# Kernel tuning notes

Measured on AMD Instinct MI355X. Metric: run time of the kernel, lower is better.

Reference implementation:

```python
import jax, jax.numpy as jnp
import numpy as np

DIM = 1024
HEADS = 16
DIM_HEAD = DIM // HEADS  # 64


def setup_inputs() -> dict:
    key = jax.random.key(0)
    k1, k2, k3 = jax.random.split(key, 3)
    x = jax.random.normal(k1, (4, 2048, DIM), dtype=jnp.float32)
    # Linear weights stored as [in, out] so y = x @ W (torch Linear uses x @ W.T; init is random either way)
    w_qkv = jax.random.normal(k2, (DIM, 3 * DIM), dtype=jnp.float32) * (DIM ** -0.5)
    w_out = jax.random.normal(k3, (DIM, DIM), dtype=jnp.float32) * (DIM ** -0.5)
    return {"x": x, "w_qkv": w_qkv, "w_out": w_out}


def reference(x, w_qkv, w_out):
    b, t, d = x.shape
    h, dh = HEADS, DIM_HEAD
    qkv = x @ w_qkv  # [b, t, 3*h*dh]
    q, k, v = jnp.split(qkv, 3, axis=-1)
    split_heads = lambda a: a.reshape(b, t, h, dh).transpose(0, 2, 1, 3)  # [b,h,t,dh]
    q, k, v = map(split_heads, (q, k, v))
    # NOTE: original scales by full model dim d, not per-head dim
    scale = d ** (-0.5)
    dots = jnp.einsum('bhie,bhje->bhij', q, k) * scale  # [b,h,t,t]
    attn = jax.nn.softmax(dots, axis=-1)
    out = jnp.einsum('bhij,bhje->bhie', attn, v)  # [b,h,t,dh]
    out = out.transpose(0, 2, 1, 3).reshape(b, t, h * dh)
    return out @ w_out
```

## Files before the change

kernel.cpp:

```cpp
#include <hip/hip_runtime.h>


typedef __bf16 bf16x8 __attribute__((ext_vector_type(8)));
typedef __bf16 bf16x4 __attribute__((ext_vector_type(4)));
typedef float f32x4 __attribute__((ext_vector_type(4)));
typedef unsigned short ushort8 __attribute__((ext_vector_type(8)));

#define MFMA16(a, b, c) __builtin_amdgcn_mfma_f32_16x16x32_bf16((a), (b), (c), 0, 0, 0)

__device__ __forceinline__ unsigned short f2bf(float f) {
  unsigned int u = __float_as_uint(f);
  u = (u + 0x7FFFu + ((u >> 16) & 1u)) >> 16;
  return (unsigned short)u;
}

__device__ __forceinline__ float fast_exp2(float x) {
#if __has_builtin(__builtin_amdgcn_exp2f)
  return __builtin_amdgcn_exp2f(x);
#else
  float r;
  asm("v_exp_f32 %0, %1" : "=v"(r) : "v"(x));
  return r;
#endif
}

__device__ __forceinline__ void gload_lds16(const unsigned short* g, unsigned short* l) {
  __builtin_amdgcn_global_load_lds(
      (const __attribute__((address_space(1))) unsigned int*)g,
      (__attribute__((address_space(3))) unsigned int*)l, 16, 0, 0);
}

__global__ __launch_bounds__(256) void cvt_f32_bf16(
    const float* __restrict__ in, unsigned short* __restrict__ out, int n) {
  int i = (blockIdx.x * 256 + threadIdx.x) * 8;
  if (i < n) {
    float4 a = *(const float4*)&in[i];
    float4 b = *(const float4*)&in[i + 4];
    ushort8 o = {f2bf(a.x), f2bf(a.y), f2bf(a.z), f2bf(a.w),
                 f2bf(b.x), f2bf(b.y), f2bf(b.z), f2bf(b.w)};
    *(ushort8*)&out[i] = o;
  }
}

__global__ __launch_bounds__(256) void transpose_f32_bf16(
    const float* __restrict__ in, unsigned short* __restrict__ out,
    int R, int C, int scale_limit, float scale) {
  __shared__ float t[32][33];
  const int c0 = blockIdx.x * 32, r0 = blockIdx.y * 32;
  const int tid = threadIdx.x;
#pragma unroll
  for (int i = 0; i < 4; ++i) {
    int e = tid + i * 256;
    int r = e >> 5, c = e & 31;
    t[r][c] = in[(size_t)(r0 + r) * C + c0 + c];
  }
  __syncthreads();
#pragma unroll
  for (int i = 0; i < 4; ++i) {
    int e = tid + i * 256;
    int r = e >> 5, c = e & 31;
    float v = t[c][r];
    if (c0 + r < scale_limit) v *= scale;
    out[(size_t)(c0 + r) * R + r0 + c] = f2bf(v);
  }
}

__global__ __launch_bounds__(256) void extract_vt(
    const unsigned short* __restrict__ qkv, unsigned short* __restrict__ VT) {
  const int bh = blockIdx.y, b = bh >> 4, h = bh & 15;
  const int t0 = blockIdx.x * 32;
  __shared__ unsigned short tile[32][65];
  const int tid = threadIdx.x;
#pragma unroll
  for (int i = 0; i < 8; ++i) {
    int e = tid + i * 256;
    int r = e >> 6, c = e & 63;
    tile[r][c] = qkv[(size_t)(b * 2048 + t0 + r) * 3072 + 2048 + h * 64 + c];
  }
  __syncthreads();
#pragma unroll
  for (int i = 0; i < 8; ++i) {
    int e = tid + i * 256;
    int r = e >> 5, c = e & 31;
    VT[(size_t)bh * 131072 + (size_t)r * 2048 + t0 + c] = tile[c][r];
  }
}

template <bool OUT_F32>
__global__ __launch_bounds__(256) void gemm_bt(
    const unsigned short* __restrict__ A, const unsigned short* __restrict__ Bt,
    void* __restrict__ Cv, int M, int N, int K) {
  __shared__ unsigned short As[128 * 32];
  __shared__ unsigned short Bs[128 * 32];
  const int tid = threadIdx.x;
  const int wave = tid >> 6, lane = tid & 63;
  const int g = lane >> 4, ln = lane & 15;
  const int wm = wave >> 1, wn = wave & 1;
  const long bm = (long)blockIdx.y * 128;
  const long bn = (long)blockIdx.x * 128;

  f32x4 acc[4][4];
#pragma unroll
  for (int i = 0; i < 4; ++i)
#pragma unroll
    for (int j = 0; j < 4; ++j) acc[i][j] = (f32x4){0.f, 0.f, 0.f, 0.f};

  const int srow = wave * 32 + (lane >> 2);
  const int scol = (lane & 3) * 8;
  const unsigned short* gA0 = A + (bm + srow) * (long)K + scol;
  const unsigned short* gA1 = gA0 + 16 * (long)K;
  const unsigned short* gB0 = Bt + (bn + srow) * (long)K + scol;
  const unsigned short* gB1 = gB0 + 16 * (long)K;
  unsigned short* lA0 = &As[wave * 1024];
  unsigned short* lA1 = &As[wave * 1024 + 512];
  unsigned short* lB0 = &Bs[wave * 1024];
  unsigned short* lB1 = &Bs[wave * 1024 + 512];

  for (int k0 = 0; k0 < K; k0 += 32) {
    __syncthreads();
    gload_lds16(gA0 + k0, lA0);
    gload_lds16(gA1 + k0, lA1);
    gload_lds16(gB0 + k0, lB0);
    gload_lds16(gB1 + k0, lB1);
    __syncthreads();

    bf16x8 af[4], bfr[4];
#pragma unroll
    for (int i = 0; i < 4; ++i) {
      af[i]  = *(const bf16x8*)&As[(wm * 64 + i * 16 + ln) * 32 + g * 8];
      bfr[i] = *(const bf16x8*)&Bs[(wn * 64 + i * 16 + ln) * 32 + g * 8];
    }
    __builtin_amdgcn_s_setprio(1);
#pragma unroll
    for (int i = 0; i < 4; ++i)
#pragma unroll
      for (int j = 0; j < 4; ++j)
        acc[i][j] = MFMA16(af[i], bfr[j], acc[i][j]);
    __builtin_amdgcn_s_setprio(0);
  }

  const long crow = bm + wm * 64, ccol = bn + wn * 64;
#pragma unroll
  for (int i = 0; i < 4; ++i)
#pragma unroll
    for (int j = 0; j < 4; ++j)
#pragma unroll
      for (int r = 0; r < 4; ++r) {
        long idx = (crow + i * 16 + g * 4 + r) * (long)N + ccol + j * 16 + ln;
        if (OUT_F32)
          ((float*)Cv)[idx] = acc[i][j][r];
        else
          ((unsigned short*)Cv)[idx] = f2bf(acc[i][j][r]);
      }
}

__global__ __launch_bounds__(256, 4) void attn_kernel(
    const unsigned short* __restrict__ qkv, const unsigned short* __restrict__ VT,
    unsigned short* __restrict__ attn_out) {
  __shared__ unsigned short Ks[64][72];
  __shared__ unsigned short Vs[64][72];
  __shared__ unsigned short Ps[4][2][16][72];

  const int tid = threadIdx.x;
  const int wave = tid >> 6, lane = tid & 63;
  const int g = lane >> 4, ln = lane & 15;

  const int wg = (blockIdx.x & 7) * 128 + (blockIdx.x >> 3);
  const int bh = wg >> 4, qc = wg & 15;
  const int b = bh >> 4, h = bh & 15;
  const int q0 = qc * 128;

  bf16x8 qf[2][2];
#pragma unroll
  for (int qb = 0; qb < 2; ++qb) {
    size_t base =
        (size_t)(b * 2048 + q0 + wave * 32 + qb * 16 + ln) * 3072 + h * 64 + g * 8;
    qf[qb][0] = *(const bf16x8*)&qkv[base];
    qf[qb][1] = *(const bf16x8*)&qkv[base + 32];
  }

  f32x4 oacc[2][4];
#pragma unroll
  for (int qb = 0; qb < 2; ++qb)
#pragma unroll
    for (int m = 0; m < 4; ++m) oacc[qb][m] = (f32x4){0.f, 0.f, 0.f, 0.f};
  float lsum[2] = {0.f, 0.f};

  const int srow = tid >> 3;
  const int sch = (tid & 7) * 8;
  const unsigned short* gK =
      qkv + (size_t)b * 2048 * 3072 + 1024 + h * 64 + (size_t)srow * 3072 + sch;
  const unsigned short* gV = VT + (size_t)bh * 131072 + (size_t)srow * 2048 + sch;

  for (int j0 = 0; j0 < 2048; j0 += 64) {
    __syncthreads();
    *(ushort8*)&Ks[srow][sch]      = *(const ushort8*)(gK + (size_t)j0 * 3072);
    *(ushort8*)&Ks[srow + 32][sch] = *(const ushort8*)(gK + (size_t)(j0 + 32) * 3072);
    *(ushort8*)&Vs[srow][sch]      = *(const ushort8*)(gV + j0);
    *(ushort8*)&Vs[srow + 32][sch] = *(const ushort8*)(gV + 32 * 2048 + j0);
    __syncthreads();

    f32x4 sacc[2][4];
#pragma unroll
    for (int qb = 0; qb < 2; ++qb)
#pragma unroll
      for (int mb = 0; mb < 4; ++mb) sacc[qb][mb] = (f32x4){0.f, 0.f, 0.f, 0.f};
    __builtin_amdgcn_s_setprio(1);
#pragma unroll
    for (int mb = 0; mb < 4; ++mb) {
      bf16x8 kf0 = *(const bf16x8*)&Ks[mb * 16 + ln][g * 8];
      bf16x8 kf1 = *(const bf16x8*)&Ks[mb * 16 + ln][32 + g * 8];
#pragma unroll
      for (int qb = 0; qb < 2; ++qb) {
        sacc[qb][mb] = MFMA16(kf0, qf[qb][0], sacc[qb][mb]);
        sacc[qb][mb] = MFMA16(kf1, qf[qb][1], sacc[qb][mb]);
      }
    }
    __builtin_amdgcn_s_setprio(0);

#pragma unroll
    for (int qb = 0; qb < 2; ++qb) {
#pragma unroll
      for (int mb = 0; mb < 4; ++mb) {
        float p0 = fast_exp2(sacc[qb][mb][0]);
        float p1 = fast_exp2(sacc[qb][mb][1]);
        float p2 = fast_exp2(sacc[qb][mb][2]);
        float p3 = fast_exp2(sacc[qb][mb][3]);
        lsum[qb] += (p0 + p1) + (p2 + p3);
        bf16x4 pk = {(__bf16)p0, (__bf16)p1, (__bf16)p2, (__bf16)p3};
        *(bf16x4*)&Ps[wave][qb][ln][mb * 16 + g * 4] = pk;
      }
    }

    asm volatile("s_waitcnt lgkmcnt(0)" ::: "memory");

    bf16x8 pf[2][2];
#pragma unroll
    for (int qb = 0; qb < 2; ++qb) {
      pf[qb][0] = *(const bf16x8*)&Ps[wave][qb][ln][g * 8];
      pf[qb][1] = *(const bf16x8*)&Ps[wave][qb][ln][32 + g * 8];
    }
    __builtin_amdgcn_s_setprio(1);
#pragma unroll
    for (int mb = 0; mb < 4; ++mb) {
      bf16x8 vf0 = *(const bf16x8*)&Vs[mb * 16 + ln][g * 8];
      bf16x8 vf1 = *(const bf16x8*)&Vs[mb * 16 + ln][32 + g * 8];
#pragma unroll
      for (int qb = 0; qb < 2; ++qb) {
        oacc[qb][mb] = MFMA16(vf0, pf[qb][0], oacc[qb][mb]);
        oacc[qb][mb] = MFMA16(vf1, pf[qb][1], oacc[qb][mb]);
      }
    }
    __builtin_amdgcn_s_setprio(0);
  }

#pragma unroll
  for (int qb = 0; qb < 2; ++qb) {
    float l = lsum[qb];
    l += __shfl_xor(l, 16);
    l += __shfl_xor(l, 32);
    float inv = 1.0f / l;
    size_t row = (size_t)(b * 2048 + q0 + wave * 32 + qb * 16 + ln) * 1024 + h * 64;
#pragma unroll
    for (int mb = 0; mb < 4; ++mb) {
      bf16x4 o = {(__bf16)(oacc[qb][mb][0] * inv), (__bf16)(oacc[qb][mb][1] * inv),
                  (__bf16)(oacc[qb][mb][2] * inv), (__bf16)(oacc[qb][mb][3] * inv)};
      *(bf16x4*)&attn_out[row + mb * 16 + g * 4] = o;
    }
  }
}

extern "C" void kernel_launch(void* const* d_in, const int* in_sizes, int n_in,
                              void* d_out, int out_size, void* d_ws, size_t ws_size,
                              hipStream_t stream) {
  (void)in_sizes; (void)n_in; (void)out_size; (void)ws_size;
  const float* x_f     = (const float*)d_in[0];
  const float* w_qkv_f = (const float*)d_in[1];
  const float* w_out_f = (const float*)d_in[2];
  float* out = (float*)d_out;

  char* ws = (char*)d_ws;
  unsigned short* qkv   = (unsigned short*)(ws);
  unsigned short* attn  = (unsigned short*)(ws + 50331648);
  unsigned short* VT    = (unsigned short*)(ws + 67108864);
  unsigned short* WqkvT = (unsigned short*)(ws + 83886080);
  unsigned short* WoutT = (unsigned short*)(ws + 90177536);
  unsigned short* xb    = (unsigned short*)(ws + 92274688);

  const float kQScale = 0.045084220027780106f;

  cvt_f32_bf16<<<4096, 256, 0, stream>>>(x_f, xb, 8192 * 1024);
  transpose_f32_bf16<<<dim3(3072 / 32, 1024 / 32), 256, 0, stream>>>(
      w_qkv_f, WqkvT, 1024, 3072, 1024, kQScale);
  transpose_f32_bf16<<<dim3(1024 / 32, 1024 / 32), 256, 0, stream>>>(
      w_out_f, WoutT, 1024, 1024, 0, 1.0f);
  gemm_bt<false><<<dim3(3072 / 128, 8192 / 128), 256, 0, stream>>>(xb, WqkvT, qkv, 8192, 3072, 1024);
  extract_vt<<<dim3(64, 64), 256, 0, stream>>>(qkv, VT);
  attn_kernel<<<1024, 256, 0, stream>>>(qkv, VT, attn);
  gemm_bt<true><<<dim3(1024 / 128, 8192 / 128), 256, 0, stream>>>(attn, WoutT, out, 8192, 1024, 1024);
}
```

Baseline: 201.0 us.

## Fuse prep kernels and write V transposed directly from QKV GEMM epilogue

Merges the x conversion and both weight transposes into a single prep kernel, and removes the separate extract_vt pass by having the QKV GEMM epilogue write the V columns straight into the transposed VT layout. This removes three kernel launches and one full read/write pass over V. The attention row-sum accumulation is also changed to packed two-wide float adds. The VT epilogue stores are 8-byte strided writes, which may be less coalesced than the original row-major stores.

```diff
diff --git a/kernel.cpp b/kernel.cpp
--- a/kernel.cpp
+++ b/kernel.cpp
@@ -4,6 +4,7 @@
 typedef __bf16 bf16x8 __attribute__((ext_vector_type(8)));
 typedef __bf16 bf16x4 __attribute__((ext_vector_type(4)));
 typedef float f32x4 __attribute__((ext_vector_type(4)));
+typedef float f32x2 __attribute__((ext_vector_type(2)));
 typedef unsigned short ushort8 __attribute__((ext_vector_type(8)));
 
 #define MFMA16(a, b, c) __builtin_amdgcn_mfma_f32_16x16x32_bf16((a), (b), (c), 0, 0, 0)
@@ -30,24 +31,35 @@
       (__attribute__((address_space(3))) unsigned int*)l, 16, 0, 0);
 }
 
-__global__ __launch_bounds__(256) void cvt_f32_bf16(
-    const float* __restrict__ in, unsigned short* __restrict__ out, int n) {
-  int i = (blockIdx.x * 256 + threadIdx.x) * 8;
-  if (i < n) {
-    float4 a = *(const float4*)&in[i];
-    float4 b = *(const float4*)&in[i + 4];
+__global__ __launch_bounds__(256) void prep_kernel(
+    const float* __restrict__ x, unsigned short* __restrict__ xb,
+    const float* __restrict__ wqkv, unsigned short* __restrict__ WqkvT,
+    const float* __restrict__ wout, unsigned short* __restrict__ WoutT) {
+  const int bid = blockIdx.x;
+  const int tid = threadIdx.x;
+  if (bid < 4096) {
+    int i = (bid * 256 + tid) * 8;
+    float4 a = *(const float4*)&x[i];
+    float4 b = *(const float4*)&x[i + 4];
     ushort8 o = {f2bf(a.x), f2bf(a.y), f2bf(a.z), f2bf(a.w),
                  f2bf(b.x), f2bf(b.y), f2bf(b.z), f2bf(b.w)};
-    *(ushort8*)&out[i] = o;
-  }
-}
-
-__global__ __launch_bounds__(256) void transpose_f32_bf16(
-    const float* __restrict__ in, unsigned short* __restrict__ out,
-    int R, int C, int scale_limit, float scale) {
+    *(ushort8*)&xb[i] = o;
+    return;
+  }
   __shared__ float t[32][33];
-  const int c0 = blockIdx.x * 32, r0 = blockIdx.y * 32;
-  const int tid = threadIdx.x;
+  const float* in;
+  unsigned short* out;
+  int C, scale_limit, c0, r0;
+  if (bid < 4096 + 3072) {
+    int tj = bid - 4096;
+    in = wqkv; out = WqkvT; C = 3072; scale_limit = 1024;
+    c0 = (tj % 96) * 32; r0 = (tj / 96) * 32;
+  } else {
+    int tj = bid - 7168;
+    in = wout; out = WoutT; C = 1024; scale_limit = 0;
+    c0 = (tj & 31) * 32; r0 = (tj >> 5) * 32;
+  }
+  const float kQScale = 0.045084220027780106f;
 #pragma unroll
   for (int i = 0; i < 4; ++i) {
     int e = tid + i * 256;
@@ -60,36 +72,16 @@
     int e = tid + i * 256;
     int r = e >> 5, c = e & 31;
     float v = t[c][r];
-    if (c0 + r < scale_limit) v *= scale;
-    out[(size_t)(c0 + r) * R + r0 + c] = f2bf(v);
-  }
-}
-
-__global__ __launch_bounds__(256) void extract_vt(
-    const unsigned short* __restrict__ qkv, unsigned short* __restrict__ VT) {
-  const int bh = blockIdx.y, b = bh >> 4, h = bh & 15;
-  const int t0 = blockIdx.x * 32;
-  __shared__ unsigned short tile[32][65];
-  const int tid = threadIdx.x;
-#pragma unroll
-  for (int i = 0; i < 8; ++i) {
-    int e = tid + i * 256;
-    int r = e >> 6, c = e & 63;
-    tile[r][c] = qkv[(size_t)(b * 2048 + t0 + r) * 3072 + 2048 + h * 64 + c];
-  }
-  __syncthreads();
-#pragma unroll
-  for (int i = 0; i < 8; ++i) {
-    int e = tid + i * 256;
-    int r = e >> 5, c = e & 31;
-    VT[(size_t)bh * 131072 + (size_t)r * 2048 + t0 + c] = tile[c][r];
-  }
-}
-
-template <bool OUT_F32>
+    if (c0 + r < scale_limit) v *= kQScale;
+    out[(size_t)(c0 + r) * 1024 + r0 + c] = f2bf(v);
+  }
+}
+
+template <int MODE>
 __global__ __launch_bounds__(256) void gemm_bt(
     const unsigned short* __restrict__ A, const unsigned short* __restrict__ Bt,
-    void* __restrict__ Cv, int M, int N, int K) {
+    void* __restrict__ Cv, unsigned short* __restrict__ VT,
+    int M, int N, int K) {
   __shared__ unsigned short As[128 * 32];
   __shared__ unsigned short Bs[128 * 32];
   const int tid = threadIdx.x;
@@ -140,18 +132,34 @@
   }
 
   const long crow = bm + wm * 64, ccol = bn + wn * 64;
-#pragma unroll
-  for (int i = 0; i < 4; ++i)
-#pragma unroll
-    for (int j = 0; j < 4; ++j)
-#pragma unroll
-      for (int r = 0; r < 4; ++r) {
-        long idx = (crow + i * 16 + g * 4 + r) * (long)N + ccol + j * 16 + ln;
-        if (OUT_F32)
-          ((float*)Cv)[idx] = acc[i][j][r];
-        else
-          ((unsigned short*)Cv)[idx] = f2bf(acc[i][j][r]);
+  if (MODE == 2 && bn >= 2048) {
+#pragma unroll
+    for (int i = 0; i < 4; ++i)
+#pragma unroll
+      for (int j = 0; j < 4; ++j) {
+        int nv = (int)(ccol + j * 16 + ln) - 2048;
+        int h = nv >> 6, dh = nv & 63;
+        long tg = crow + i * 16 + g * 4;
+        int b = (int)(tg >> 11), tl = (int)(tg & 2047);
+        size_t idx = (size_t)(b * 16 + h) * 131072 + (size_t)dh * 2048 + tl;
+        bf16x4 o = {(__bf16)acc[i][j][0], (__bf16)acc[i][j][1],
+                    (__bf16)acc[i][j][2], (__bf16)acc[i][j][3]};
+        *(bf16x4*)&VT[idx] = o;
       }
+  } else {
+#pragma unroll
+    for (int i = 0; i < 4; ++i)
+#pragma unroll
+      for (int j = 0; j < 4; ++j)
+#pragma unroll
+        for (int r = 0; r < 4; ++r) {
+          long idx = (crow + i * 16 + g * 4 + r) * (long)N + ccol + j * 16 + ln;
+          if (MODE == 1)
+            ((float*)Cv)[idx] = acc[i][j][r];
+          else
+            ((unsigned short*)Cv)[idx] = f2bf(acc[i][j][r]);
+        }
+  }
 }
 
 __global__ __launch_bounds__(256, 4) void attn_kernel(
@@ -184,7 +192,7 @@
   for (int qb = 0; qb < 2; ++qb)
 #pragma unroll
     for (int m = 0; m < 4; ++m) oacc[qb][m] = (f32x4){0.f, 0.f, 0.f, 0.f};
-  float lsum[2] = {0.f, 0.f};
+  f32x2 ls[2] = {(f32x2){0.f, 0.f}, (f32x2){0.f, 0.f}};
 
   const int srow = tid >> 3;
   const int sch = (tid & 7) * 8;
@@ -226,7 +234,7 @@
         float p1 = fast_exp2(sacc[qb][mb][1]);
         float p2 = fast_exp2(sacc[qb][mb][2]);
         float p3 = fast_exp2(sacc[qb][mb][3]);
-        lsum[qb] += (p0 + p1) + (p2 + p3);
+        ls[qb] += (f32x2){p0, p1} + (f32x2){p2, p3};
         bf16x4 pk = {(__bf16)p0, (__bf16)p1, (__bf16)p2, (__bf16)p3};
         *(bf16x4*)&Ps[wave][qb][ln][mb * 16 + g * 4] = pk;
       }
@@ -256,7 +264,7 @@
 
 #pragma unroll
   for (int qb = 0; qb < 2; ++qb) {
-    float l = lsum[qb];
+    float l = ls[qb].x + ls[qb].y;
     l += __shfl_xor(l, 16);
     l += __shfl_xor(l, 32);
     float inv = 1.0f / l;
@@ -287,15 +295,8 @@
   unsigned short* WoutT = (unsigned short*)(ws + 90177536);
   unsigned short* xb    = (unsigned short*)(ws + 92274688);
 
-  const float kQScale = 0.045084220027780106f;
-
-  cvt_f32_bf16<<<4096, 256, 0, stream>>>(x_f, xb, 8192 * 1024);
-  transpose_f32_bf16<<<dim3(3072 / 32, 1024 / 32), 256, 0, stream>>>(
-      w_qkv_f, WqkvT, 1024, 3072, 1024, kQScale);
-  transpose_f32_bf16<<<dim3(1024 / 32, 1024 / 32), 256, 0, stream>>>(
-      w_out_f, WoutT, 1024, 1024, 0, 1.0f);
-  gemm_bt<false><<<dim3(3072 / 128, 8192 / 128), 256, 0, stream>>>(xb, WqkvT, qkv, 8192, 3072, 1024);
-  extract_vt<<<dim3(64, 64), 256, 0, stream>>>(qkv, VT);
+  prep_kernel<<<8192, 256, 0, stream>>>(x_f, xb, w_qkv_f, WqkvT, w_out_f, WoutT);
+  gemm_bt<2><<<dim3(24, 64), 256, 0, stream>>>(xb, WqkvT, qkv, VT, 8192, 3072, 1024);
   attn_kernel<<<1024, 256, 0, stream>>>(qkv, VT, attn);
-  gemm_bt<true><<<dim3(1024 / 128, 8192 / 128), 256, 0, stream>>>(attn, WoutT, out, 8192, 1024, 1024);
-}
+  gemm_bt<1><<<dim3(8, 64), 256, 0, stream>>>(attn, WoutT, out, nullptr, 8192, 1024, 1024);
+}
```

Result: faster. 193.5 us (-3.7%).
